# Kernel optimization log

Hardware: AMD Instinct MI355X
Metric: run time of the kernel (lower is better)

Reference implementation:

```python
import jax, jax.numpy as jnp
import numpy as np

N = 50000   # nodes
E = 800000  # edges (before self-loops)
D = 128     # d_model == in_dim
H = 8       # heads
C = D // H  # per-head channels = 16
NEG_SLOPE = 0.2  # PyG GATConv default


def gat_conv(x, row, col, W, a_src, a_dst, bias):
    # x: [N, Din]; row/col: [E'] src/dst with self-loops; W: [Din, H*C]
    h = (x @ W).reshape(N, H, C)                       # [N, H, C]
    alpha_src = (h * a_src).sum(-1)                    # [N, H]
    alpha_dst = (h * a_dst).sum(-1)                    # [N, H]
    e = jax.nn.leaky_relu(alpha_src[row] + alpha_dst[col], NEG_SLOPE)  # [E', H]
    # segment softmax over incoming edges of each dst node (col)
    e_max = jax.ops.segment_max(e, col, num_segments=N)               # [N, H]
    e_exp = jnp.exp(e - e_max[col])                                   # [E', H]
    denom = jax.ops.segment_sum(e_exp, col, num_segments=N)           # [N, H]
    alpha = e_exp / (denom[col] + 1e-16)                              # [E', H]
    msg = h[row] * alpha[:, :, None]                                  # [E', H, C]
    out = jax.ops.segment_sum(msg, col, num_segments=N)               # [N, H, C]
    return out.reshape(N, H * C) + bias


def setup_inputs() -> dict:
    key = jax.random.key(0)
    ks = jax.random.split(key, 14)
    s = 0.05
    return {
        "x": jax.random.normal(ks[0], (N, D), dtype=jnp.float32),
        "edge_index": jax.random.randint(ks[1], (2, E), 0, N, dtype=jnp.int64),
        "pos": jax.random.normal(ks[2], (N, 3), dtype=jnp.float32),
        "W1": jax.random.normal(ks[3], (D, H * C), dtype=jnp.float32) * s,
        "a_src1": jax.random.normal(ks[4], (H, C), dtype=jnp.float32) * s,
        "a_dst1": jax.random.normal(ks[5], (H, C), dtype=jnp.float32) * s,
        "b1": jnp.zeros((H * C,), dtype=jnp.float32),
        "W2": jax.random.normal(ks[6], (D, H * C), dtype=jnp.float32) * s,
        "a_src2": jax.random.normal(ks[7], (H, C), dtype=jnp.float32) * s,
        "a_dst2": jax.random.normal(ks[8], (H, C), dtype=jnp.float32) * s,
        "b2": jnp.zeros((H * C,), dtype=jnp.float32),
        "Wd": jax.random.normal(ks[9], (1, D), dtype=jnp.float32) * s,
        "bd": jnp.zeros((D,), dtype=jnp.float32),
    }


def reference(x, edge_index, pos, W1, a_src1, a_dst1, b1, W2, a_src2, a_dst2, b2, Wd, bd):
    row, col = edge_index[0], edge_index[1]
    # dist embedding (computed in source forward, not used in the returned sum)
    dist = jnp.linalg.norm(pos[row] - pos[col], axis=1, keepdims=True)  # [E, 1]
    dist_emb = jax.nn.relu(dist @ Wd + bd)  # noqa: F841 (unused, as in source)
    # GATConv adds self-loops internally (PyG default add_self_loops=True)
    loop = jnp.arange(N, dtype=row.dtype)
    row_sl = jnp.concatenate([row, loop])
    col_sl = jnp.concatenate([col, loop])
    h1 = jax.nn.relu(gat_conv(x, row_sl, col_sl, W1, a_src1, a_dst1, b1))
    h2 = jax.nn.relu(gat_conv(h1, row_sl, col_sl, W2, a_src2, a_dst2, b2))
    return x + h1 + h2
```

## Files before the change

### kernel.cpp

```cpp
#include <hip/hip_runtime.h>
#include <hip/hip_bf16.h>
#include <math.h>


constexpr int D = 128;
constexpr int CAP = 64;
constexpr int WPACK = 18432;
constexpr int NBMAX = 64;
constexpr int BCAP = 24576;
constexpr int EPB = 4096;

using bf16x8 = __attribute__((ext_vector_type(8))) short;
using f32x4 = __attribute__((ext_vector_type(4))) float;

static __device__ __forceinline__ float lrelu(float v) {
  return v > 0.f ? v : 0.2f * v;
}

static __device__ __forceinline__ ushort bfbits(float f) {
  __hip_bfloat16 b = __float2bfloat16(f);
  return *reinterpret_cast<ushort*>(&b);
}

static __device__ __forceinline__ float bf2f(ushort u) {
  union { unsigned int u; float f; } c;
  c.u = (unsigned int)u << 16;
  return c.f;
}

__global__ void pack_all_kernel(const float* __restrict__ W1, const float* __restrict__ as1,
                                const float* __restrict__ ad1, ushort* __restrict__ wp1,
                                const float* __restrict__ W2, const float* __restrict__ as2,
                                const float* __restrict__ ad2, ushort* __restrict__ wp2,
                                int* __restrict__ bucket_cnt) {
  int t = blockIdx.x * blockDim.x + threadIdx.x;
  if (t < NBMAX) bucket_cnt[t] = 0;
  const float *W, *as_, *ad_;
  ushort* wp;
  int idx;
  if (t < WPACK) {
    W = W1; as_ = as1; ad_ = ad1; wp = wp1; idx = t;
  } else if (t < 2 * WPACK) {
    W = W2; as_ = as2; ad_ = ad2; wp = wp2; idx = t - WPACK;
  } else {
    return;
  }
  if (idx < 16384) {
    int e = idx & 7, c = (idx >> 3) & 15, ct = (idx >> 7) & 7, g = (idx >> 10) & 3,
        ks = idx >> 12;
    int k = ks * 32 + g * 8 + e, n = ct * 16 + c;
    wp[idx] = bfbits(W[k * 128 + n]);
  } else {
    int j = idx - 16384;
    int e = j & 7, c = (j >> 3) & 15, g = (j >> 7) & 3, ks = j >> 9;
    int k = ks * 32 + g * 8 + e;
    int h = c & 7;
    const float* a = (c >> 3) ? ad_ : as_;
    float s = 0.f;
    #pragma unroll
    for (int cc = 0; cc < 16; ++cc) s += W[k * 128 + h * 16 + cc] * a[h * 16 + cc];
    wp[idx] = bfbits(s);
  }
}

__global__ __launch_bounds__(256) void bucket_kernel(
    const int* __restrict__ row, const int* __restrict__ col,
    int* __restrict__ bucket_cnt, unsigned int* __restrict__ bkt, int E, int NB) {
  __shared__ int hist[NBMAX];
  __shared__ int base_s[NBMAX];
  int tid = threadIdx.x;
  if (tid < NBMAX) hist[tid] = 0;
  __syncthreads();
  int e0 = blockIdx.x * EPB;
  unsigned int uv[16];
  int bb[16], rr[16];
  #pragma unroll
  for (int j = 0; j < 16; ++j) {
    int e = e0 + j * 256 + tid;
    bb[j] = -1; uv[j] = 0; rr[j] = 0;
    if (e < E) {
      int c = col[e], r = row[e];
      bb[j] = c >> 10;
      uv[j] = ((unsigned int)(c & 1023) << 16) | (unsigned int)r;
      rr[j] = atomicAdd(&hist[bb[j]], 1);
    }
  }
  __syncthreads();
  if (tid < NB) base_s[tid] = atomicAdd(&bucket_cnt[tid], hist[tid]);
  __syncthreads();
  #pragma unroll
  for (int j = 0; j < 16; ++j) {
    if (bb[j] >= 0) {
      int pos = base_s[bb[j]] + rr[j];
      if (pos < BCAP) bkt[(size_t)bb[j] * BCAP + pos] = uv[j];
    }
  }
}

__global__ __launch_bounds__(256) void csr_gemm_kernel(
    const float* __restrict__ X, const ushort* __restrict__ Wp,
    ushort* __restrict__ Hf, ushort* __restrict__ asrc, float* __restrict__ adst,
    int N, const unsigned int* __restrict__ bkt, const int* __restrict__ bucket_cnt,
    int* __restrict__ cnt, ushort* __restrict__ csr_pad, int NB) {
  __shared__ ushort Wl[WPACK];
  int tid = threadIdx.x;
  if ((int)blockIdx.x < NB) {
    int b = blockIdx.x;
    int* lcnt = (int*)Wl;
    for (int i = tid; i < 1024; i += 256) lcnt[i] = 0;
    __syncthreads();
    int ce = min(bucket_cnt[b], BCAP);
    const unsigned int* bp = bkt + (size_t)b * BCAP;
    for (int i = tid; i < ce; i += 256) {
      unsigned int u = bp[i];
      int dl = u >> 16;
      int p = atomicAdd(&lcnt[dl], 1);
      if (p < CAP) csr_pad[((size_t)((b << 10) + dl)) * CAP + p] = (ushort)(u & 0xffffu);
    }
    __syncthreads();
    int nd = min(1024, N - (b << 10));
    for (int i = tid; i < nd; i += 256) cnt[(b << 10) + i] = lcnt[i];
    return;
  }

  for (int i = tid; i < WPACK / 8; i += 256)
    *(uint4*)&Wl[i * 8] = *(const uint4*)&Wp[i * 8];
  __syncthreads();

  int lane = tid & 63, w = tid >> 6;
  int g = lane >> 4, c = lane & 15;
  int rt0 = ((int)blockIdx.x - NB) * 128 + w * 32;

  f32x4 acc[2][9];
  #pragma unroll
  for (int rt = 0; rt < 2; ++rt)
    #pragma unroll
    for (int ct = 0; ct < 9; ++ct) acc[rt][ct] = (f32x4)0.f;

  #pragma unroll
  for (int ks = 0; ks < 4; ++ks) {
    bf16x8 a[2];
    #pragma unroll
    for (int rt = 0; rt < 2; ++rt) {
      int r = rt0 + rt * 16 + c;
      if (r < N) {
        const float* xp = &X[(size_t)r * D + ks * 32 + g * 8];
        float4 x0 = *(const float4*)xp;
        float4 x1 = *(const float4*)(xp + 4);
        bf16x8 t;
        t[0] = (short)bfbits(x0.x); t[1] = (short)bfbits(x0.y);
        t[2] = (short)bfbits(x0.z); t[3] = (short)bfbits(x0.w);
        t[4] = (short)bfbits(x1.x); t[5] = (short)bfbits(x1.y);
        t[6] = (short)bfbits(x1.z); t[7] = (short)bfbits(x1.w);
        a[rt] = t;
      } else {
        a[rt] = (bf16x8)(short)0;
      }
    }
    #pragma unroll
    for (int ct = 0; ct < 9; ++ct) {
      const ushort* bp = (ct < 8)
          ? &Wl[(size_t)(((ks * 4 + g) * 8 + ct) * 16 + c) * 8]
          : &Wl[16384 + (size_t)((ks * 4 + g) * 16 + c) * 8];
      bf16x8 b = *(const bf16x8*)bp;
      acc[0][ct] = __builtin_amdgcn_mfma_f32_16x16x32_bf16(a[0], b, acc[0][ct], 0, 0, 0);
      acc[1][ct] = __builtin_amdgcn_mfma_f32_16x16x32_bf16(a[1], b, acc[1][ct], 0, 0, 0);
    }
  }

  #pragma unroll
  for (int rt = 0; rt < 2; ++rt) {
    #pragma unroll
    for (int j = 0; j < 4; ++j) {
      int r = rt0 + rt * 16 + g * 4 + j;
      if (r >= N) continue;
      #pragma unroll
      for (int ct = 0; ct < 8; ++ct)
        Hf[(size_t)r * D + ct * 16 + c] = bfbits(acc[rt][ct][j]);
      float lv = acc[rt][8][j];
      if (c < 8) asrc[r * 8 + c] = bfbits(lv);
      else adst[r * 8 + (c - 8)] = lv;
    }
  }
}

__global__ __launch_bounds__(256) void gemm2_kernel(
    const ushort* __restrict__ Xv, const ushort* __restrict__ Wp,
    ushort* __restrict__ Hf, ushort* __restrict__ asrc, float* __restrict__ adst,
    int N) {
  __shared__ ushort Wl[WPACK];
  int tid = threadIdx.x;
  for (int i = tid; i < WPACK / 8; i += 256)
    *(uint4*)&Wl[i * 8] = *(const uint4*)&Wp[i * 8];
  __syncthreads();

  int lane = tid & 63, w = tid >> 6;
  int g = lane >> 4, c = lane & 15;
  int rt0 = blockIdx.x * 128 + w * 32;

  f32x4 acc[2][9];
  #pragma unroll
  for (int rt = 0; rt < 2; ++rt)
    #pragma unroll
    for (int ct = 0; ct < 9; ++ct) acc[rt][ct] = (f32x4)0.f;

  #pragma unroll
  for (int ks = 0; ks < 4; ++ks) {
    bf16x8 a[2];
    #pragma unroll
    for (int rt = 0; rt < 2; ++rt) {
      int r = rt0 + rt * 16 + c;
      a[rt] = (r < N) ? *(const bf16x8*)&Xv[(size_t)r * D + ks * 32 + g * 8]
                      : (bf16x8)(short)0;
    }
    #pragma unroll
    for (int ct = 0; ct < 9; ++ct) {
      const ushort* bp = (ct < 8)
          ? &Wl[(size_t)(((ks * 4 + g) * 8 + ct) * 16 + c) * 8]
          : &Wl[16384 + (size_t)((ks * 4 + g) * 16 + c) * 8];
      bf16x8 b = *(const bf16x8*)bp;
      acc[0][ct] = __builtin_amdgcn_mfma_f32_16x16x32_bf16(a[0], b, acc[0][ct], 0, 0, 0);
      acc[1][ct] = __builtin_amdgcn_mfma_f32_16x16x32_bf16(a[1], b, acc[1][ct], 0, 0, 0);
    }
  }

  #pragma unroll
  for (int rt = 0; rt < 2; ++rt) {
    #pragma unroll
    for (int j = 0; j < 4; ++j) {
      int r = rt0 + rt * 16 + g * 4 + j;
      if (r >= N) continue;
      #pragma unroll
      for (int ct = 0; ct < 8; ++ct)
        Hf[(size_t)r * D + ct * 16 + c] = bfbits(acc[rt][ct][j]);
      float lv = acc[rt][8][j];
      if (c < 8) asrc[r * 8 + c] = bfbits(lv);
      else adst[r * 8 + (c - 8)] = lv;
    }
  }
}

static __device__ __forceinline__ void gather_node(
    const ushort* __restrict__ Hf, const ushort* __restrict__ asrc, float adst_h,
    const int* __restrict__ cnt, const ushort* __restrict__ csr_pad,
    int dst, int h, int d0, float& accx, float& accy, float& wsum) {
  float ws = __expf(lrelu(bf2f(asrc[dst * 8 + h]) + adst_h));
  ushort2 fs = *(const ushort2*)&Hf[(size_t)dst * D + d0];
  accx = ws * bf2f(fs.x); accy = ws * bf2f(fs.y); wsum = ws;
  int cn = min(cnt[dst], CAP);
  const ushort* cp = csr_pad + (size_t)dst * CAP;
  int i = 0;
  for (; i + 8 <= cn; i += 8) {
    ushort4 sa = *(const ushort4*)(cp + i);
    ushort4 sb = *(const ushort4*)(cp + i + 4);
    int s[8] = {sa.x, sa.y, sa.z, sa.w, sb.x, sb.y, sb.z, sb.w};
    float l[8];
    ushort2 f[8];
    #pragma unroll
    for (int j = 0; j < 8; ++j) l[j] = bf2f(asrc[s[j] * 8 + h]);
    #pragma unroll
    for (int j = 0; j < 8; ++j) f[j] = *(const ushort2*)&Hf[(size_t)s[j] * D + d0];
    #pragma unroll
    for (int j = 0; j < 8; ++j) {
      float we = __expf(lrelu(l[j] + adst_h));
      accx += we * bf2f(f[j].x);
      accy += we * bf2f(f[j].y);
      wsum += we;
    }
  }
  for (; i + 4 <= cn; i += 4) {
    ushort4 s4 = *(const ushort4*)(cp + i);
    int s[4] = {s4.x, s4.y, s4.z, s4.w};
    float l[4];
    ushort2 f[4];
    #pragma unroll
    for (int j = 0; j < 4; ++j) l[j] = bf2f(asrc[s[j] * 8 + h]);
    #pragma unroll
    for (int j = 0; j < 4; ++j) f[j] = *(const ushort2*)&Hf[(size_t)s[j] * D + d0];
    #pragma unroll
    for (int j = 0; j < 4; ++j) {
      float we = __expf(lrelu(l[j] + adst_h));
      accx += we * bf2f(f[j].x);
      accy += we * bf2f(f[j].y);
      wsum += we;
    }
  }
  for (; i < cn; ++i) {
    int src = cp[i];
    float we = __expf(lrelu(bf2f(asrc[src * 8 + h]) + adst_h));
    ushort2 fv = *(const ushort2*)&Hf[(size_t)src * D + d0];
    accx += we * bf2f(fv.x);
    accy += we * bf2f(fv.y);
    wsum += we;
  }
}

template <int LAYER>
__global__ __launch_bounds__(256) void aggregate_kernel(
    const ushort* __restrict__ Hf, const ushort* __restrict__ asrc,
    const float* __restrict__ adst, const int* __restrict__ cnt,
    const ushort* __restrict__ csr_pad, const float* __restrict__ bias,
    const float* __restrict__ xin, const ushort* __restrict__ h1in,
    void* __restrict__ outp, int N) {
  int wid = (blockIdx.x * blockDim.x + threadIdx.x) >> 6;
  if (wid >= N) return;
  int lane = threadIdx.x & 63;
  int h = lane >> 3, d0 = lane * 2;
  int dst = wid;
  float adh = adst[dst * 8 + h];
  float ax, ay, wsm;
  gather_node(Hf, asrc, adh, cnt, csr_pad, dst, h, d0, ax, ay, wsm);
  float inv = 1.f / (wsm + 1e-16f);
  float2 bv = *(const float2*)&bias[d0];
  float r0 = fmaxf(ax * inv + bv.x, 0.f);
  float r1 = fmaxf(ay * inv + bv.y, 0.f);
  if (LAYER == 1) {
    ushort2 u;
    u.x = bfbits(r0); u.y = bfbits(r1);
    *(ushort2*)&((ushort*)outp)[(size_t)dst * D + d0] = u;
  } else {
    float2 xv = *(const float2*)&xin[(size_t)dst * D + d0];
    ushort2 hv = *(const ushort2*)&h1in[(size_t)dst * D + d0];
    *(float2*)&((float*)outp)[(size_t)dst * D + d0] =
        make_float2(xv.x + bf2f(hv.x) + r0, xv.y + bf2f(hv.y) + r1);
  }
}

extern "C" void kernel_launch(void* const* d_in, const int* in_sizes, int n_in,
                              void* d_out, int out_size, void* d_ws, size_t ws_size,
                              hipStream_t stream) {
  const float* x = (const float*)d_in[0];
  const int* ei = (const int*)d_in[1];
  const float* W1 = (const float*)d_in[3];
  const float* as1 = (const float*)d_in[4];
  const float* ad1 = (const float*)d_in[5];
  const float* b1 = (const float*)d_in[6];
  const float* W2 = (const float*)d_in[7];
  const float* as2 = (const float*)d_in[8];
  const float* ad2 = (const float*)d_in[9];
  const float* b2 = (const float*)d_in[10];
  float* out = (float*)d_out;

  const int N = in_sizes[0] / D;
  const int E = in_sizes[1] / 2;
  const int* row = ei;
  const int* col = ei + E;
  const int NB = (N + 1023) >> 10;

  char* base = (char*)d_ws;
  size_t o = 0;
  auto alloc = [&](size_t bytes) {
    void* p = base + o;
    o = (o + bytes + 255) & ~(size_t)255;
    return p;
  };
  int* bucket_cnt = (int*)alloc((size_t)NBMAX * 4);
  unsigned int* bkt = (unsigned int*)alloc((size_t)NBMAX * BCAP * 4);
  int* cnt = (int*)alloc((size_t)N * 4);
  ushort* csr_pad = (ushort*)alloc((size_t)N * CAP * 2);
  ushort* hf = (ushort*)alloc((size_t)N * D * 2);
  ushort* h1 = (ushort*)alloc((size_t)N * D * 2);
  ushort* asrcb = (ushort*)alloc((size_t)N * 8 * 2);
  float* adstb = (float*)alloc((size_t)N * 8 * 4);
  ushort* wp1 = (ushort*)alloc((size_t)WPACK * 2);
  ushort* wp2 = (ushort*)alloc((size_t)WPACK * 2);

  int gemm_blocks = (N + 127) / 128;
  int agg_blocks = (N + 3) / 4;

  pack_all_kernel<<<(2 * WPACK + 255) / 256, 256, 0, stream>>>(
      W1, as1, ad1, wp1, W2, as2, ad2, wp2, bucket_cnt);
  bucket_kernel<<<(E + EPB - 1) / EPB, 256, 0, stream>>>(row, col, bucket_cnt, bkt, E, NB);
  csr_gemm_kernel<<<NB + gemm_blocks, 256, 0, stream>>>(
      x, wp1, hf, asrcb, adstb, N, bkt, bucket_cnt, cnt, csr_pad, NB);
  aggregate_kernel<1><<<agg_blocks, 256, 0, stream>>>(
      hf, asrcb, adstb, cnt, csr_pad, b1, nullptr, nullptr, h1, N);
  gemm2_kernel<<<gemm_blocks, 256, 0, stream>>>(h1, wp2, hf, asrcb, adstb, N);
  aggregate_kernel<2><<<agg_blocks, 256, 0, stream>>>(
      hf, asrcb, adstb, cnt, csr_pad, b2, x, h1, out, N);
}
```

Baseline: 230.4 us.

## Split each node's edge list across two half-wavefronts with 8-byte feature loads

The aggregation kernel now splits each 64-lane wavefront into two halves of 32 lanes. Each half handles alternating edges of the destination node, and each lane loads four bf16 channels (8 bytes) per source row instead of two. The two halves' partial sums are combined with a cross-half shuffle before normalisation and the epilogue. This puts two independent gathers in flight per wavefront and widens the loads to cut per-edge instruction overhead. In exchange it adds a reduction shuffle and leaves half the lanes idle during the epilogue.

```diff
diff --git a/kernel.cpp b/kernel.cpp
--- a/kernel.cpp
+++ b/kernel.cpp
@@ -240,61 +240,6 @@
   }
 }
 
-static __device__ __forceinline__ void gather_node(
-    const ushort* __restrict__ Hf, const ushort* __restrict__ asrc, float adst_h,
-    const int* __restrict__ cnt, const ushort* __restrict__ csr_pad,
-    int dst, int h, int d0, float& accx, float& accy, float& wsum) {
-  float ws = __expf(lrelu(bf2f(asrc[dst * 8 + h]) + adst_h));
-  ushort2 fs = *(const ushort2*)&Hf[(size_t)dst * D + d0];
-  accx = ws * bf2f(fs.x); accy = ws * bf2f(fs.y); wsum = ws;
-  int cn = min(cnt[dst], CAP);
-  const ushort* cp = csr_pad + (size_t)dst * CAP;
-  int i = 0;
-  for (; i + 8 <= cn; i += 8) {
-    ushort4 sa = *(const ushort4*)(cp + i);
-    ushort4 sb = *(const ushort4*)(cp + i + 4);
-    int s[8] = {sa.x, sa.y, sa.z, sa.w, sb.x, sb.y, sb.z, sb.w};
-    float l[8];
-    ushort2 f[8];
-    #pragma unroll
-    for (int j = 0; j < 8; ++j) l[j] = bf2f(asrc[s[j] * 8 + h]);
-    #pragma unroll
-    for (int j = 0; j < 8; ++j) f[j] = *(const ushort2*)&Hf[(size_t)s[j] * D + d0];
-    #pragma unroll
-    for (int j = 0; j < 8; ++j) {
-      float we = __expf(lrelu(l[j] + adst_h));
-      accx += we * bf2f(f[j].x);
-      accy += we * bf2f(f[j].y);
-      wsum += we;
-    }
-  }
-  for (; i + 4 <= cn; i += 4) {
-    ushort4 s4 = *(const ushort4*)(cp + i);
-    int s[4] = {s4.x, s4.y, s4.z, s4.w};
-    float l[4];
-    ushort2 f[4];
-    #pragma unroll
-    for (int j = 0; j < 4; ++j) l[j] = bf2f(asrc[s[j] * 8 + h]);
-    #pragma unroll
-    for (int j = 0; j < 4; ++j) f[j] = *(const ushort2*)&Hf[(size_t)s[j] * D + d0];
-    #pragma unroll
-    for (int j = 0; j < 4; ++j) {
-      float we = __expf(lrelu(l[j] + adst_h));
-      accx += we * bf2f(f[j].x);
-      accy += we * bf2f(f[j].y);
-      wsum += we;
-    }
-  }
-  for (; i < cn; ++i) {
-    int src = cp[i];
-    float we = __expf(lrelu(bf2f(asrc[src * 8 + h]) + adst_h));
-    ushort2 fv = *(const ushort2*)&Hf[(size_t)src * D + d0];
-    accx += we * bf2f(fv.x);
-    accy += we * bf2f(fv.y);
-    wsum += we;
-  }
-}
-
 template <int LAYER>
 __global__ __launch_bounds__(256) void aggregate_kernel(
     const ushort* __restrict__ Hf, const ushort* __restrict__ asrc,
@@ -305,24 +250,72 @@
   int wid = (blockIdx.x * blockDim.x + threadIdx.x) >> 6;
   if (wid >= N) return;
   int lane = threadIdx.x & 63;
-  int h = lane >> 3, d0 = lane * 2;
+  int g = lane >> 5;
+  int q = lane & 31;
+  int c0 = q * 4;
+  int h = q >> 2;
   int dst = wid;
   float adh = adst[dst * 8 + h];
-  float ax, ay, wsm;
-  gather_node(Hf, asrc, adh, cnt, csr_pad, dst, h, d0, ax, ay, wsm);
-  float inv = 1.f / (wsm + 1e-16f);
-  float2 bv = *(const float2*)&bias[d0];
-  float r0 = fmaxf(ax * inv + bv.x, 0.f);
-  float r1 = fmaxf(ay * inv + bv.y, 0.f);
-  if (LAYER == 1) {
-    ushort2 u;
-    u.x = bfbits(r0); u.y = bfbits(r1);
-    *(ushort2*)&((ushort*)outp)[(size_t)dst * D + d0] = u;
-  } else {
-    float2 xv = *(const float2*)&xin[(size_t)dst * D + d0];
-    ushort2 hv = *(const ushort2*)&h1in[(size_t)dst * D + d0];
-    *(float2*)&((float*)outp)[(size_t)dst * D + d0] =
-        make_float2(xv.x + bf2f(hv.x) + r0, xv.y + bf2f(hv.y) + r1);
+  float a0 = 0.f, a1 = 0.f, a2 = 0.f, a3 = 0.f, wsum = 0.f;
+  if (g == 0) {
+    float ws = __expf(lrelu(bf2f(asrc[dst * 8 + h]) + adh));
+    ushort4 fs = *(const ushort4*)&Hf[(size_t)dst * D + c0];
+    a0 = ws * bf2f(fs.x); a1 = ws * bf2f(fs.y);
+    a2 = ws * bf2f(fs.z); a3 = ws * bf2f(fs.w);
+    wsum = ws;
+  }
+  int cn = min(cnt[dst], CAP);
+  const ushort* cp = csr_pad + (size_t)dst * CAP;
+  int i = 0;
+  for (; i + 8 <= cn; i += 8) {
+    ushort4 s4 = *(const ushort4*)(cp + i + g * 4);
+    int s[4] = {s4.x, s4.y, s4.z, s4.w};
+    float l[4];
+    ushort4 f[4];
+    #pragma unroll
+    for (int j = 0; j < 4; ++j) l[j] = bf2f(asrc[s[j] * 8 + h]);
+    #pragma unroll
+    for (int j = 0; j < 4; ++j) f[j] = *(const ushort4*)&Hf[(size_t)s[j] * D + c0];
+    #pragma unroll
+    for (int j = 0; j < 4; ++j) {
+      float we = __expf(lrelu(l[j] + adh));
+      a0 += we * bf2f(f[j].x); a1 += we * bf2f(f[j].y);
+      a2 += we * bf2f(f[j].z); a3 += we * bf2f(f[j].w);
+      wsum += we;
+    }
+  }
+  for (int j = i + g; j < cn; j += 2) {
+    int s = cp[j];
+    float we = __expf(lrelu(bf2f(asrc[s * 8 + h]) + adh));
+    ushort4 fv = *(const ushort4*)&Hf[(size_t)s * D + c0];
+    a0 += we * bf2f(fv.x); a1 += we * bf2f(fv.y);
+    a2 += we * bf2f(fv.z); a3 += we * bf2f(fv.w);
+    wsum += we;
+  }
+  a0 += __shfl_xor(a0, 32); a1 += __shfl_xor(a1, 32);
+  a2 += __shfl_xor(a2, 32); a3 += __shfl_xor(a3, 32);
+  wsum += __shfl_xor(wsum, 32);
+  if (g == 0) {
+    float inv = 1.f / (wsum + 1e-16f);
+    float4 bv = *(const float4*)&bias[c0];
+    float r0 = fmaxf(a0 * inv + bv.x, 0.f);
+    float r1 = fmaxf(a1 * inv + bv.y, 0.f);
+    float r2 = fmaxf(a2 * inv + bv.z, 0.f);
+    float r3 = fmaxf(a3 * inv + bv.w, 0.f);
+    if (LAYER == 1) {
+      ushort4 u;
+      u.x = bfbits(r0); u.y = bfbits(r1); u.z = bfbits(r2); u.w = bfbits(r3);
+      *(ushort4*)&((ushort*)outp)[(size_t)dst * D + c0] = u;
+    } else {
+      float4 xv = *(const float4*)&xin[(size_t)dst * D + c0];
+      ushort4 hv = *(const ushort4*)&h1in[(size_t)dst * D + c0];
+      float4 ov;
+      ov.x = xv.x + bf2f(hv.x) + r0;
+      ov.y = xv.y + bf2f(hv.y) + r1;
+      ov.z = xv.z + bf2f(hv.z) + r2;
+      ov.w = xv.w + bf2f(hv.w) + r3;
+      *(float4*)&((float*)outp)[(size_t)dst * D + c0] = ov;
+    }
   }
 }
 
```

Measured after the change: 233.2 us. About the same (+1.2%).
